# Optimization experiments

Hardware: AMD Instinct MI355X
Metric: run time of the kernel (lower is better)

Reference implementation:

```python
import jax, jax.numpy as jnp
import numpy as np
import math

B, S, D, H, DFF, L = 8, 1024, 512, 8, 2048, 4
DK = D // H
EPS = 1e-5
NEG = -1e32


def _sinusoidal_pe(s, d):
    pos = np.arange(s)[:, None].astype(np.float32)
    div = np.exp(np.arange(0, d, 2).astype(np.float32) * (-math.log(10000.0) / d))
    pe = np.zeros((s, d), np.float32)
    pe[:, 0::2] = np.sin(pos * div)
    pe[:, 1::2] = np.cos(pos * div)
    return jnp.asarray(pe)


def setup_inputs() -> dict:
    key = jax.random.key(0)
    ks = jax.random.split(key, 20)
    sd = 0.02
    inp = {
        "q_embed_data": jax.random.normal(ks[0], (B, S, D), jnp.float32),
        "qa_embed_data": jax.random.normal(ks[1], (B, S, D), jnp.float32),
        "pe": _sinusoidal_pe(S, D),
        # stacked per-layer params (leading dim L). kq_same=1 -> q uses Wk.
        "Wk": sd * jax.random.normal(ks[2], (L, D, D), jnp.float32),
        "bk": jnp.zeros((L, D), jnp.float32),
        "Wv": sd * jax.random.normal(ks[3], (L, D, D), jnp.float32),
        "bv": jnp.zeros((L, D), jnp.float32),
        "Wo": sd * jax.random.normal(ks[4], (L, D, D), jnp.float32),
        "bo": jnp.zeros((L, D), jnp.float32),
        "ln1_s": jnp.ones((L, D), jnp.float32),
        "ln1_b": jnp.zeros((L, D), jnp.float32),
        "W1": sd * jax.random.normal(ks[5], (L, D, DFF), jnp.float32),
        "b1": jnp.zeros((L, DFF), jnp.float32),
        "W2": sd * jax.random.normal(ks[6], (L, DFF, D), jnp.float32),
        "b2": jnp.zeros((L, D), jnp.float32),
        "ln2_s": jnp.ones((L, D), jnp.float32),
        "ln2_b": jnp.zeros((L, D), jnp.float32),
    }
    return inp


def _layernorm(z, s, b):
    m = z.mean(-1, keepdims=True)
    v = ((z - m) ** 2).mean(-1, keepdims=True)
    return (z - m) / jnp.sqrt(v + EPS) * s + b


def _forward(q_embed_data, qa_embed_data, pe, Wk, bk, Wv, bv, Wo, bo,
             ln1_s, ln1_b, W1, b1, W2, b2, ln2_s, ln2_b):
    x = q_embed_data + pe[None, :, :]
    y = qa_embed_data + pe[None, :, :]  # values source stays fixed across blocks
    allowed = jnp.tril(jnp.ones((S, S), bool), -1)  # strictly-causal: attend only to j < i
    row_keep = (jnp.arange(S) > 0).astype(x.dtype)[None, None, :, None]  # zero_pad row 0

    def heads(z, W, b):
        return (z @ W + b).reshape(B, S, H, DK).transpose(0, 2, 1, 3)  # [B,H,S,DK]

    def step(xc, p):
        wk, bk_, wv, bv_, wo, bo_, s1, b1n, w1, b1f, w2, b2f, s2, b2n = p
        q = heads(xc, wk, bk_)  # kq_same: q via k_linear
        k = heads(xc, wk, bk_)
        v = heads(y, wv, bv_)
        sc = jnp.einsum('bhid,bhjd->bhij', q, k) / math.sqrt(DK)
        att = jax.nn.softmax(jnp.where(allowed, sc, NEG), axis=-1) * row_keep
        o = jnp.einsum('bhij,bhjd->bhid', att, v).transpose(0, 2, 1, 3).reshape(B, S, D)
        x1 = _layernorm(xc + (o @ wo + bo_), s1, b1n)
        f = jax.nn.relu(x1 @ w1 + b1f) @ w2 + b2f
        x2 = _layernorm(x1 + f, s2, b2n)
        return x2, None

    out, _ = jax.lax.scan(step, x, (Wk, bk, Wv, bv, Wo, bo, ln1_s, ln1_b, W1, b1, W2, b2, ln2_s, ln2_b))
    return out


def reference(q_embed_data, qa_embed_data, pe, Wk, bk, Wv, bv, Wo, bo,
              ln1_s, ln1_b, W1, b1, W2, b2, ln2_s, ln2_b):
    return _forward(q_embed_data, qa_embed_data, pe, Wk, bk, Wv, bv, Wo, bo,
                    ln1_s, ln1_b, W1, b1, W2, b2, ln2_s, ln2_b)
```

## Files before the change

### kernel.cpp

```cpp
#include <hip/hip_runtime.h>
#include <stdint.h>

typedef __attribute__((ext_vector_type(8))) __bf16 bf16x8;
typedef __attribute__((ext_vector_type(4))) float f32x4;
typedef __attribute__((ext_vector_type(4))) unsigned int u32x4;

constexpr int B = 8, S = 1024, D = 512, H = 8, DFF = 2048, L = 4, DK = 64;
constexpr int MR = B * S;

__device__ __forceinline__ unsigned short f2bf(float f) {
    union { float f; unsigned u; } v; v.f = f;
    unsigned u = v.u;
    u += 0x7fffu + ((u >> 16) & 1u);
    return (unsigned short)(u >> 16);
}

__device__ __forceinline__ void gload_lds16(const void* g, void* l) {
    __builtin_amdgcn_global_load_lds(
        (const __attribute__((address_space(1))) void*)g,
        (__attribute__((address_space(3))) void*)l, 16, 0, 0);
}

__global__ __launch_bounds__(256) void add_pe_kernel(
    const float* __restrict__ qe, const float* __restrict__ qa,
    const float* __restrict__ pe, float* __restrict__ x_f32,
    unsigned short* __restrict__ x_bf, unsigned short* __restrict__ y_bf) {
    int gid = blockIdx.x * 256 + threadIdx.x;
    int base = gid * 4;
    int po = base & (S * D - 1);
    float4 p = *(const float4*)(pe + po);
    float4 a = *(const float4*)(qe + base);
    float4 q = *(const float4*)(qa + base);
    float4 xv = make_float4(a.x + p.x, a.y + p.y, a.z + p.z, a.w + p.w);
    float4 yv = make_float4(q.x + p.x, q.y + p.y, q.z + p.z, q.w + p.w);
    *(float4*)(x_f32 + base) = xv;
    ushort4 xb; xb.x = f2bf(xv.x); xb.y = f2bf(xv.y); xb.z = f2bf(xv.z); xb.w = f2bf(xv.w);
    ushort4 yb; yb.x = f2bf(yv.x); yb.y = f2bf(yv.y); yb.z = f2bf(yv.z); yb.w = f2bf(yv.w);
    *(ushort4*)(x_bf + base) = xb;
    *(ushort4*)(y_bf + base) = yb;
}

__global__ __launch_bounds__(256) void wtrans_kernel(
    const float* __restrict__ src, unsigned short* __restrict__ dst, int K, int N) {
    __shared__ float t[64][65];
    src += (size_t)blockIdx.z * K * N;
    dst += (size_t)blockIdx.z * K * N;
    int n0 = blockIdx.x * 64, k0 = blockIdx.y * 64;
    int tid = threadIdx.x;
    int r = tid >> 4, c4 = (tid & 15) * 4;
    #pragma unroll
    for (int rr = 0; rr < 64; rr += 16) {
        float4 v = *(const float4*)(src + (size_t)(k0 + r + rr) * N + n0 + c4);
        t[r + rr][c4] = v.x; t[r + rr][c4 + 1] = v.y;
        t[r + rr][c4 + 2] = v.z; t[r + rr][c4 + 3] = v.w;
    }
    __syncthreads();
    int n = tid >> 2, kc = (tid & 3) * 16;
    ushort4 o[4];
    #pragma unroll
    for (int g = 0; g < 4; g++) {
        o[g].x = f2bf(t[kc + g * 4 + 0][n]);
        o[g].y = f2bf(t[kc + g * 4 + 1][n]);
        o[g].z = f2bf(t[kc + g * 4 + 2][n]);
        o[g].w = f2bf(t[kc + g * 4 + 3][n]);
    }
    unsigned short* dp = dst + (size_t)(n0 + n) * K + k0 + kc;
    #pragma unroll
    for (int g = 0; g < 4; g++) *(ushort4*)(dp + g * 4) = o[g];
}

template<int BN, bool RELU, bool RESID, bool OUT_F32, bool OUT_BF16, bool OUT_VT>
__global__ __launch_bounds__(256) void gemm_kernel(
    const unsigned short* __restrict__ A, const unsigned short* __restrict__ Bt,
    const float* __restrict__ bias, const float* __restrict__ resid,
    float* __restrict__ out_f32, unsigned short* __restrict__ out_bf,
    int M, int N, int K) {
    constexpr int MT = (BN == 128) ? 4 : 2;
    constexpr int WROWS = (BN == 128) ? 64 : 32;
    __shared__ unsigned short a_lds[128 * 32];
    __shared__ unsigned short b_lds[BN * 32];

    const int tid = threadIdx.x;
    const int lane = tid & 63, wid = tid >> 6;
    const int wm = (BN == 128) ? (wid >> 1) : wid;
    const int wn = (BN == 128) ? (wid & 1) : 0;
    const int l15 = lane & 15, quad = lane >> 4;
    const int m0 = blockIdx.x * 128, n0 = blockIdx.y * BN;

    f32x4 acc[MT][4];
    #pragma unroll
    for (int i = 0; i < MT; i++)
        #pragma unroll
        for (int j = 0; j < 4; j++) { f32x4 z = {0.f, 0.f, 0.f, 0.f}; acc[i][j] = z; }

    const int c0 = wid * 128 + lane, c1 = c0 + 64;
    const int r0 = c0 >> 2, kga0 = (c0 & 3) ^ ((r0 >> 1) & 3);
    const int r1 = c1 >> 2, kga1 = (c1 & 3) ^ ((r1 >> 1) & 3);
    const unsigned short* aP0 = A + (size_t)(m0 + r0) * K + kga0 * 8;
    const unsigned short* aP1 = A + (size_t)(m0 + r1) * K + kga1 * 8;
    unsigned short* aL0 = a_lds + wid * 1024;
    unsigned short* aL1 = aL0 + 512;

    const unsigned short *bP0, *bP1;
    unsigned short *bL0, *bL1;
    if (BN == 128) {
        bP0 = Bt + (size_t)(n0 + r0) * K + kga0 * 8;
        bP1 = Bt + (size_t)(n0 + r1) * K + kga1 * 8;
        bL0 = b_lds + wid * 1024;
        bL1 = bL0 + 512;
    } else {
        int cb = tid, rb = cb >> 2, kgb = (cb & 3) ^ ((rb >> 1) & 3);
        bP0 = Bt + (size_t)(n0 + rb) * K + kgb * 8;
        bP1 = nullptr;
        bL0 = b_lds + wid * 512;
        bL1 = nullptr;
    }

    for (int k0 = 0; k0 < K; k0 += 32) {
        gload_lds16(aP0 + k0, aL0);
        gload_lds16(aP1 + k0, aL1);
        gload_lds16(bP0 + k0, bL0);
        if (BN == 128) gload_lds16(bP1 + k0, bL1);
        __syncthreads();

        bf16x8 af[MT], bfv[4];
        #pragma unroll
        for (int mt = 0; mt < MT; mt++) {
            int row = wm * WROWS + mt * 16 + l15;
            af[mt] = *(const bf16x8*)&a_lds[row * 32 + ((quad ^ ((row >> 1) & 3)) * 8)];
        }
        #pragma unroll
        for (int nt = 0; nt < 4; nt++) {
            int row = wn * 64 + nt * 16 + l15;
            bfv[nt] = *(const bf16x8*)&b_lds[row * 32 + ((quad ^ ((row >> 1) & 3)) * 8)];
        }
        #pragma unroll
        for (int mt = 0; mt < MT; mt++)
            #pragma unroll
            for (int nt = 0; nt < 4; nt++)
                acc[mt][nt] = __builtin_amdgcn_mfma_f32_16x16x32_bf16(af[mt], bfv[nt], acc[mt][nt], 0, 0, 0);
        __syncthreads();
    }

    #pragma unroll
    for (int nt = 0; nt < 4; nt++) {
        int col = n0 + wn * 64 + nt * 16 + l15;
        float bv = bias[col];
        #pragma unroll
        for (int mt = 0; mt < MT; mt++) {
            int row0 = m0 + wm * WROWS + mt * 16 + quad * 4;
            if (OUT_VT) {
                int hh = col >> 6, d = col & 63;
                int bb = row0 >> 10, s0 = row0 & 1023;
                ushort4 o;
                o.x = f2bf(acc[mt][nt][0] + bv);
                o.y = f2bf(acc[mt][nt][1] + bv);
                o.z = f2bf(acc[mt][nt][2] + bv);
                o.w = f2bf(acc[mt][nt][3] + bv);
                *(ushort4*)(out_bf + ((size_t)(bb * H + hh) * DK + d) * S + s0) = o;
            } else {
                #pragma unroll
                for (int r = 0; r < 4; r++) {
                    int row = row0 + r;
                    float v = acc[mt][nt][r] + bv;
                    if (RESID) v += resid[(size_t)row * N + col];
                    if (RELU) v = fmaxf(v, 0.f);
                    size_t o = (size_t)row * N + col;
                    if (OUT_F32) out_f32[o] = v;
                    if (OUT_BF16) out_bf[o] = f2bf(v);
                }
            }
        }
    }
}

__global__ __launch_bounds__(256) void ln_kernel(
    const float* __restrict__ in, const float* __restrict__ gamma,
    const float* __restrict__ beta, float* __restrict__ out_f32,
    unsigned short* __restrict__ out_bf) {
    __shared__ float red[8];
    int row = blockIdx.x, tid = threadIdx.x;
    const float* p = in + (size_t)row * D;
    float2 v = *(const float2*)(p + tid * 2);
    float s = v.x + v.y;
    float q = v.x * v.x + v.y * v.y;
    #pragma unroll
    for (int off = 32; off > 0; off >>= 1) {
        s += __shfl_xor(s, off);
        q += __shfl_xor(q, off);
    }
    int wid = tid >> 6, lane = tid & 63;
    if (lane == 0) { red[wid] = s; red[4 + wid] = q; }
    __syncthreads();
    s = red[0] + red[1] + red[2] + red[3];
    q = red[4] + red[5] + red[6] + red[7];
    float mean = s * (1.f / D);
    float var = q * (1.f / D) - mean * mean;
    float inv = rsqrtf(var + 1e-5f);
    int c = tid * 2;
    float2 g = *(const float2*)(gamma + c);
    float2 bb = *(const float2*)(beta + c);
    float o0 = (v.x - mean) * inv * g.x + bb.x;
    float o1 = (v.y - mean) * inv * g.y + bb.y;
    *(float2*)(out_f32 + (size_t)row * D + c) = make_float2(o0, o1);
    ushort2 ob; ob.x = f2bf(o0); ob.y = f2bf(o1);
    *(ushort2*)(out_bf + (size_t)row * D + c) = ob;
}

__device__ __forceinline__ void load_kfrag(const unsigned short* kbase, int kt,
                                           int l15, int quad, bf16x8 (&kf)[4][2]) {
    #pragma unroll
    for (int mt = 0; mt < 4; mt++) {
        const unsigned short* kr = kbase + (size_t)(kt * 64 + mt * 16 + l15) * D;
        kf[mt][0] = *(const bf16x8*)(kr + quad * 8);
        kf[mt][1] = *(const bf16x8*)(kr + 32 + quad * 8);
    }
}
__device__ __forceinline__ void load_vfrag(const unsigned short* vbase, int kt,
                                           int l15, int quad, bf16x8 (&vf)[4][2]) {
    #pragma unroll
    for (int mt = 0; mt < 4; mt++) {
        const unsigned short* vr = vbase + (size_t)(mt * 16 + l15) * S + kt * 64;
        vf[mt][0] = *(const bf16x8*)(vr + quad * 8);
        vf[mt][1] = *(const bf16x8*)(vr + 32 + quad * 8);
    }
}

__global__ __launch_bounds__(64, 2) void attn_part_kernel(
    const unsigned short* __restrict__ qk, const unsigned short* __restrict__ vt,
    float* __restrict__ part_o, float* __restrict__ part_ml) {
    __shared__ unsigned short p_lds[32 * 72];

    int bx = blockIdx.x;
    int slot = 47 - (bx >> 6);
    int head = bx & 63;
    int b = head >> 3, h = head & 7;
    int lane = threadIdx.x;
    int l15 = lane & 15, quad = lane >> 4;

    int t, ck0, ck1;
    if (slot < 16)      { t = slot;      ck0 = 0;       ck1 = (t >> 1) + 1; }
    else if (slot < 32) { t = slot;      int nt = (t >> 1) + 1; ck0 = 0;       ck1 = nt >> 1; }
    else                { t = slot - 16; int nt = (t >> 1) + 1; ck0 = nt >> 1; ck1 = nt; }

    const int rowbase = b * S, colbase = h * DK;
    const unsigned short* kbase = qk + (size_t)rowbase * D + colbase;
    const unsigned short* vbase = vt + (size_t)(b * H + h) * (DK * S);

    bf16x8 qf[2][2];
    #pragma unroll
    for (int u = 0; u < 2; u++) {
        const unsigned short* qrow =
            qk + (size_t)(rowbase + t * 32 + u * 16 + l15) * D + colbase;
        qf[u][0] = *(const bf16x8*)(qrow + quad * 8);
        qf[u][1] = *(const bf16x8*)(qrow + 32 + quad * 8);
    }

    float m_r[2] = {-1e30f, -1e30f}, l_r[2] = {0.f, 0.f};
    f32x4 o_acc[2][4];
    #pragma unroll
    for (int u = 0; u < 2; u++)
        #pragma unroll
        for (int i = 0; i < 4; i++) { f32x4 z = {0.f, 0.f, 0.f, 0.f}; o_acc[u][i] = z; }

    auto process = [&](int kt, bf16x8 (&kf)[4][2], bf16x8 (&vf)[4][2]) {
        #pragma unroll
        for (int u = 0; u < 2; u++) {
            const int qbase = t * 32 + u * 16;
            if (kt * 64 >= qbase + 16) continue;
            const int gi = qbase + l15;

            f32x4 s_acc[4];
            #pragma unroll
            for (int mt = 0; mt < 4; mt++) {
                if (kt * 64 + mt * 16 < qbase + 16) {
                    f32x4 a = {0.f, 0.f, 0.f, 0.f};
                    a = __builtin_amdgcn_mfma_f32_16x16x32_bf16(kf[mt][0], qf[u][0], a, 0, 0, 0);
                    a = __builtin_amdgcn_mfma_f32_16x16x32_bf16(kf[mt][1], qf[u][1], a, 0, 0, 0);
                    s_acc[mt] = a;
                }
            }

            float p[4][4];
            float mx = -1e30f;
            #pragma unroll
            for (int mt = 0; mt < 4; mt++) {
                if (kt * 64 + mt * 16 < qbase + 16) {
                    #pragma unroll
                    for (int r = 0; r < 4; r++) {
                        int gj = kt * 64 + mt * 16 + quad * 4 + r;
                        float val = s_acc[mt][r] * 0.125f;
                        if (gj >= gi) val = -1e30f;
                        p[mt][r] = val;
                        mx = fmaxf(mx, val);
                    }
                }
            }
            mx = fmaxf(mx, __shfl_xor(mx, 16));
            mx = fmaxf(mx, __shfl_xor(mx, 32));
            float m_new = fmaxf(m_r[u], mx);
            float alpha = __expf(m_r[u] - m_new);
            float ls = 0.f;
            #pragma unroll
            for (int mt = 0; mt < 4; mt++) {
                bool live = kt * 64 + mt * 16 < qbase + 16;
                #pragma unroll
                for (int r = 0; r < 4; r++) {
                    float pv = live ? __expf(p[mt][r] - m_new) : 0.f;
                    p[mt][r] = pv;
                    ls += pv;
                }
            }
            ls += __shfl_xor(ls, 16);
            ls += __shfl_xor(ls, 32);
            l_r[u] = l_r[u] * alpha + ls;
            m_r[u] = m_new;

            const int ql = u * 16 + l15;
            #pragma unroll
            for (int mt = 0; mt < 4; mt++) {
                uint2 w;
                w.x = (unsigned)f2bf(p[mt][0]) | ((unsigned)f2bf(p[mt][1]) << 16);
                w.y = (unsigned)f2bf(p[mt][2]) | ((unsigned)f2bf(p[mt][3]) << 16);
                *(uint2*)&p_lds[ql * 72 + mt * 16 + quad * 4] = w;
            }
            bf16x8 pb0 = *(const bf16x8*)&p_lds[ql * 72 + quad * 8];
            bf16x8 pb1 = *(const bf16x8*)&p_lds[ql * 72 + 32 + quad * 8];

            #pragma unroll
            for (int mt = 0; mt < 4; mt++)
                #pragma unroll
                for (int r = 0; r < 4; r++)
                    o_acc[u][mt][r] *= alpha;
            #pragma unroll
            for (int mt = 0; mt < 4; mt++) {
                o_acc[u][mt] = __builtin_amdgcn_mfma_f32_16x16x32_bf16(vf[mt][0], pb0, o_acc[u][mt], 0, 0, 0);
                o_acc[u][mt] = __builtin_amdgcn_mfma_f32_16x16x32_bf16(vf[mt][1], pb1, o_acc[u][mt], 0, 0, 0);
            }
        }
    };

    bf16x8 ka[4][2], kb[4][2], va[4][2];
    load_kfrag(kbase, ck0, l15, quad, ka);
    int kt = ck0;
    while (true) {
        load_vfrag(vbase, kt, l15, quad, va);
        if (kt + 1 < ck1) load_kfrag(kbase, kt + 1, l15, quad, kb);
        process(kt, ka, va);
        if (++kt >= ck1) break;
        load_vfrag(vbase, kt, l15, quad, va);
        if (kt + 1 < ck1) load_kfrag(kbase, kt + 1, l15, quad, ka);
        process(kt, kb, va);
        if (++kt >= ck1) break;
    }

    int p = head * 48 + slot;
    if (quad == 0) {
        #pragma unroll
        for (int u = 0; u < 2; u++) {
            part_ml[(size_t)p * 64 + u * 16 + l15] = m_r[u];
            part_ml[(size_t)p * 64 + 32 + u * 16 + l15] = l_r[u];
        }
    }
    float* po = part_o + (size_t)p * 2048;
    #pragma unroll
    for (int u = 0; u < 2; u++)
        #pragma unroll
        for (int mt = 0; mt < 4; mt++)
            #pragma unroll
            for (int r = 0; r < 4; r++)
                po[(mt * 16 + quad * 4 + r) * 32 + u * 16 + l15] = o_acc[u][mt][r];
}

__global__ __launch_bounds__(256) void attn_combine_kernel(
    const float* __restrict__ part_o, const float* __restrict__ part_ml,
    unsigned short* __restrict__ ob) {
    int bx = blockIdx.x;
    int t = bx & 31, head = bx >> 5;
    int b = head >> 3, h = head & 7;
    int tid = threadIdx.x;
    int q = tid >> 3, dg = (tid & 7) * 8;
    int p0 = head * 48 + t;
    bool two = (t >= 16);
    int p1 = head * 48 + t + 16;

    float m0 = part_ml[(size_t)p0 * 64 + q];
    float l0 = part_ml[(size_t)p0 * 64 + 32 + q];
    float w0 = 1.f, w1 = 0.f, ldenom = l0;
    if (two) {
        float m1 = part_ml[(size_t)p1 * 64 + q];
        float l1 = part_ml[(size_t)p1 * 64 + 32 + q];
        float M = fmaxf(m0, m1);
        w0 = __expf(m0 - M);
        w1 = __expf(m1 - M);
        ldenom = l0 * w0 + l1 * w1;
    }
    float inv = (ldenom > 0.f) ? 1.f / ldenom : 0.f;
    int si = t * 32 + q;
    if (si == 0) inv = 0.f;

    const float* po0 = part_o + (size_t)p0 * 2048;
    const float* po1 = part_o + (size_t)p1 * 2048;
    unsigned short out[8];
    #pragma unroll
    for (int i = 0; i < 8; i++) {
        int d = dg + i;
        float v = po0[d * 32 + q] * w0;
        if (two) v += po1[d * 32 + q] * w1;
        out[i] = f2bf(v * inv);
    }
    unsigned short* dst = ob + (size_t)(b * S + si) * D + h * DK + dg;
    *(u32x4*)dst = *(const u32x4*)out;
}

extern "C" void kernel_launch(void* const* d_in, const int* in_sizes, int n_in,
                              void* d_out, int out_size, void* d_ws, size_t ws_size,
                              hipStream_t stream) {
    (void)in_sizes; (void)n_in; (void)out_size; (void)ws_size;
    const float* qe  = (const float*)d_in[0];
    const float* qa  = (const float*)d_in[1];
    const float* pe  = (const float*)d_in[2];
    const float* Wk  = (const float*)d_in[3];
    const float* bk  = (const float*)d_in[4];
    const float* Wv  = (const float*)d_in[5];
    const float* bv  = (const float*)d_in[6];
    const float* Wo  = (const float*)d_in[7];
    const float* bo  = (const float*)d_in[8];
    const float* l1s = (const float*)d_in[9];
    const float* l1b = (const float*)d_in[10];
    const float* W1  = (const float*)d_in[11];
    const float* b1  = (const float*)d_in[12];
    const float* W2  = (const float*)d_in[13];
    const float* b2  = (const float*)d_in[14];
    const float* l2s = (const float*)d_in[15];
    const float* l2b = (const float*)d_in[16];

    char* w = (char*)d_ws;
    float* x_f32  = (float*)w;           w += (size_t)MR * D * 4;
    float* t_f32  = (float*)w;           w += (size_t)MR * D * 4;
    float* x1_f32 = (float*)w;           w += (size_t)MR * D * 4;
    unsigned short* x_bf  = (unsigned short*)w; w += (size_t)MR * D * 2;
    unsigned short* y_bf  = (unsigned short*)w; w += (size_t)MR * D * 2;
    unsigned short* qk_bf = (unsigned short*)w; w += (size_t)MR * D * 2;
    unsigned short* vt_bf = (unsigned short*)w; w += (size_t)MR * D * 2;
    unsigned short* o_bf  = (unsigned short*)w; w += (size_t)MR * D * 2;
    unsigned short* x1_bf = (unsigned short*)w; w += (size_t)MR * D * 2;
    unsigned short* h_bf  = (unsigned short*)w; w += (size_t)MR * DFF * 2;
    unsigned short* wkT = (unsigned short*)w;   w += (size_t)L * D * D * 2;
    unsigned short* wvT = (unsigned short*)w;   w += (size_t)L * D * D * 2;
    unsigned short* woT = (unsigned short*)w;   w += (size_t)L * D * D * 2;
    unsigned short* w1T = (unsigned short*)w;   w += (size_t)L * D * DFF * 2;
    unsigned short* w2T = (unsigned short*)w;   w += (size_t)L * DFF * D * 2;
    float* part_o  = (float*)w;                 w += (size_t)3072 * 2048 * 4;
    float* part_ml = (float*)w;                 w += (size_t)3072 * 64 * 4;

    add_pe_kernel<<<MR * D / 4 / 256, 256, 0, stream>>>(qe, qa, pe, x_f32, x_bf, y_bf);
    wtrans_kernel<<<dim3(8, 8, L), 256, 0, stream>>>(Wk, wkT, D, D);
    wtrans_kernel<<<dim3(8, 8, L), 256, 0, stream>>>(Wv, wvT, D, D);
    wtrans_kernel<<<dim3(8, 8, L), 256, 0, stream>>>(Wo, woT, D, D);
    wtrans_kernel<<<dim3(32, 8, L), 256, 0, stream>>>(W1, w1T, D, DFF);
    wtrans_kernel<<<dim3(8, 32, L), 256, 0, stream>>>(W2, w2T, DFF, D);

    dim3 g512(64, 8), g2048(64, 16);
    for (int l = 0; l < L; l++) {
        gemm_kernel<64, false, false, false, true, false><<<g512, 256, 0, stream>>>(
            x_bf, wkT + (size_t)l * D * D, bk + l * D, nullptr, nullptr, qk_bf, MR, D, D);
        gemm_kernel<64, false, false, false, false, true><<<g512, 256, 0, stream>>>(
            y_bf, wvT + (size_t)l * D * D, bv + l * D, nullptr, nullptr, vt_bf, MR, D, D);
        attn_part_kernel<<<48 * 64, 64, 0, stream>>>(qk_bf, vt_bf, part_o, part_ml);
        attn_combine_kernel<<<64 * 32, 256, 0, stream>>>(part_o, part_ml, o_bf);
        gemm_kernel<64, false, true, true, false, false><<<g512, 256, 0, stream>>>(
            o_bf, woT + (size_t)l * D * D, bo + l * D, x_f32, t_f32, nullptr, MR, D, D);
        ln_kernel<<<MR, 256, 0, stream>>>(t_f32, l1s + l * D, l1b + l * D, x1_f32, x1_bf);
        gemm_kernel<128, true, false, false, true, false><<<g2048, 256, 0, stream>>>(
            x1_bf, w1T + (size_t)l * D * DFF, b1 + l * DFF, nullptr, nullptr, h_bf, MR, DFF, D);
        gemm_kernel<64, false, true, true, false, false><<<g512, 256, 0, stream>>>(
            h_bf, w2T + (size_t)l * DFF * D, b2 + l * D, x1_f32, t_f32, nullptr, MR, D, DFF);
        float* xo = (l == L - 1) ? (float*)d_out : x_f32;
        ln_kernel<<<MR, 256, 0, stream>>>(t_f32, l2s + l * D, l2b + l * D, xo, x_bf);
    }
}
```

Measured before the change: 875.5 us.

## Double GEMM K-tile to 64 and streamline attention softmax with exp2

The GEMM now stages 64-wide K slices per iteration with an 8-way XOR swizzle, halving barrier and loop overhead per MFMA. The attention kernel computes softmax in the base-2 domain with a folded scale and skips causal masking on off-diagonal tiles. It also packs probabilities to bf16 by truncation while accumulating the row sum from those truncated values. This doubles GEMM LDS usage and slightly changes rounding of attention probabilities.

Measured after the change: 835.3 us. 1.05x faster.

```diff
diff --git a/kernel.cpp b/kernel.cpp
--- a/kernel.cpp
+++ b/kernel.cpp
@@ -77,8 +77,9 @@
     int M, int N, int K) {
     constexpr int MT = (BN == 128) ? 4 : 2;
     constexpr int WROWS = (BN == 128) ? 64 : 32;
-    __shared__ unsigned short a_lds[128 * 32];
-    __shared__ unsigned short b_lds[BN * 32];
+    constexpr int BRND = (BN == 128) ? 4 : 2;
+    __shared__ unsigned short a_lds[128 * 64];
+    __shared__ unsigned short b_lds[BN * 64];
 
     const int tid = threadIdx.x;
     const int lane = tid & 63, wid = tid >> 6;
@@ -93,52 +94,54 @@
         #pragma unroll
         for (int j = 0; j < 4; j++) { f32x4 z = {0.f, 0.f, 0.f, 0.f}; acc[i][j] = z; }
 
-    const int c0 = wid * 128 + lane, c1 = c0 + 64;
-    const int r0 = c0 >> 2, kga0 = (c0 & 3) ^ ((r0 >> 1) & 3);
-    const int r1 = c1 >> 2, kga1 = (c1 & 3) ^ ((r1 >> 1) & 3);
-    const unsigned short* aP0 = A + (size_t)(m0 + r0) * K + kga0 * 8;
-    const unsigned short* aP1 = A + (size_t)(m0 + r1) * K + kga1 * 8;
-    unsigned short* aL0 = a_lds + wid * 1024;
-    unsigned short* aL1 = aL0 + 512;
-
-    const unsigned short *bP0, *bP1;
-    unsigned short *bL0, *bL1;
-    if (BN == 128) {
-        bP0 = Bt + (size_t)(n0 + r0) * K + kga0 * 8;
-        bP1 = Bt + (size_t)(n0 + r1) * K + kga1 * 8;
-        bL0 = b_lds + wid * 1024;
-        bL1 = bL0 + 512;
-    } else {
-        int cb = tid, rb = cb >> 2, kgb = (cb & 3) ^ ((rb >> 1) & 3);
-        bP0 = Bt + (size_t)(n0 + rb) * K + kgb * 8;
-        bP1 = nullptr;
-        bL0 = b_lds + wid * 512;
-        bL1 = nullptr;
-    }
-
-    for (int k0 = 0; k0 < K; k0 += 32) {
-        gload_lds16(aP0 + k0, aL0);
-        gload_lds16(aP1 + k0, aL1);
-        gload_lds16(bP0 + k0, bL0);
-        if (BN == 128) gload_lds16(bP1 + k0, bL1);
+    const unsigned short* aP[4];
+    unsigned short* aL[4];
+    #pragma unroll
+    for (int j = 0; j < 4; j++) {
+        int c = wid * 256 + j * 64 + lane;
+        int r = c >> 3, slot = c & 7, kg = slot ^ (r & 7);
+        aP[j] = A + (size_t)(m0 + r) * K + kg * 8;
+        aL[j] = a_lds + (size_t)(wid * 256 + j * 64) * 8;
+    }
+    const unsigned short* bP[BRND];
+    unsigned short* bL[BRND];
+    #pragma unroll
+    for (int j = 0; j < BRND; j++) {
+        int c = wid * (BRND * 64) + j * 64 + lane;
+        int r = c >> 3, slot = c & 7, kg = slot ^ (r & 7);
+        bP[j] = Bt + (size_t)(n0 + r) * K + kg * 8;
+        bL[j] = b_lds + (size_t)(wid * (BRND * 64) + j * 64) * 8;
+    }
+
+    for (int k0 = 0; k0 < K; k0 += 64) {
+        #pragma unroll
+        for (int j = 0; j < 4; j++) gload_lds16(aP[j] + k0, aL[j]);
+        #pragma unroll
+        for (int j = 0; j < BRND; j++) gload_lds16(bP[j] + k0, bL[j]);
         __syncthreads();
 
-        bf16x8 af[MT], bfv[4];
+        bf16x8 af[MT][2], bfv[4][2];
         #pragma unroll
         for (int mt = 0; mt < MT; mt++) {
             int row = wm * WROWS + mt * 16 + l15;
-            af[mt] = *(const bf16x8*)&a_lds[row * 32 + ((quad ^ ((row >> 1) & 3)) * 8)];
+            #pragma unroll
+            for (int kh = 0; kh < 2; kh++)
+                af[mt][kh] = *(const bf16x8*)&a_lds[row * 64 + (((kh * 4 + quad) ^ (row & 7)) * 8)];
         }
         #pragma unroll
         for (int nt = 0; nt < 4; nt++) {
             int row = wn * 64 + nt * 16 + l15;
-            bfv[nt] = *(const bf16x8*)&b_lds[row * 32 + ((quad ^ ((row >> 1) & 3)) * 8)];
+            #pragma unroll
+            for (int kh = 0; kh < 2; kh++)
+                bfv[nt][kh] = *(const bf16x8*)&b_lds[row * 64 + (((kh * 4 + quad) ^ (row & 7)) * 8)];
         }
         #pragma unroll
         for (int mt = 0; mt < MT; mt++)
             #pragma unroll
-            for (int nt = 0; nt < 4; nt++)
-                acc[mt][nt] = __builtin_amdgcn_mfma_f32_16x16x32_bf16(af[mt], bfv[nt], acc[mt][nt], 0, 0, 0);
+            for (int nt = 0; nt < 4; nt++) {
+                acc[mt][nt] = __builtin_amdgcn_mfma_f32_16x16x32_bf16(af[mt][0], bfv[nt][0], acc[mt][nt], 0, 0, 0);
+                acc[mt][nt] = __builtin_amdgcn_mfma_f32_16x16x32_bf16(af[mt][1], bfv[nt][1], acc[mt][nt], 0, 0, 0);
+            }
         __syncthreads();
     }
 
@@ -229,7 +232,9 @@
 __global__ __launch_bounds__(64, 2) void attn_part_kernel(
     const unsigned short* __restrict__ qk, const unsigned short* __restrict__ vt,
     float* __restrict__ part_o, float* __restrict__ part_ml) {
-    __shared__ unsigned short p_lds[32 * 72];
+    __shared__ unsigned p_u32[32 * 36];
+    constexpr float C = 0.18033688011112042f;
+    const float NEGINF = -__builtin_huge_valf();
 
     int bx = blockIdx.x;
     int slot = 47 - (bx >> 6);
@@ -263,81 +268,100 @@
         #pragma unroll
         for (int i = 0; i < 4; i++) { f32x4 z = {0.f, 0.f, 0.f, 0.f}; o_acc[u][i] = z; }
 
-    auto process = [&](int kt, bf16x8 (&kf)[4][2], bf16x8 (&vf)[4][2]) {
+    auto process = [&](int kt, bf16x8 (&kf)[4][2], bf16x8 (&vf)[4][2], bool diag) {
+        f32x4 s[2][4];
         #pragma unroll
         for (int u = 0; u < 2; u++) {
-            const int qbase = t * 32 + u * 16;
-            if (kt * 64 >= qbase + 16) continue;
-            const int gi = qbase + l15;
-
-            f32x4 s_acc[4];
+            const int qb = t * 32 + u * 16;
             #pragma unroll
             for (int mt = 0; mt < 4; mt++) {
-                if (kt * 64 + mt * 16 < qbase + 16) {
+                if (!diag || (kt * 64 + mt * 16 < qb + 16)) {
                     f32x4 a = {0.f, 0.f, 0.f, 0.f};
                     a = __builtin_amdgcn_mfma_f32_16x16x32_bf16(kf[mt][0], qf[u][0], a, 0, 0, 0);
                     a = __builtin_amdgcn_mfma_f32_16x16x32_bf16(kf[mt][1], qf[u][1], a, 0, 0, 0);
-                    s_acc[mt] = a;
+                    s[u][mt] = a;
+                } else {
+                    f32x4 a = {NEGINF, NEGINF, NEGINF, NEGINF};
+                    s[u][mt] = a;
                 }
             }
-
-            float p[4][4];
-            float mx = -1e30f;
-            #pragma unroll
-            for (int mt = 0; mt < 4; mt++) {
-                if (kt * 64 + mt * 16 < qbase + 16) {
+        }
+        if (diag) {
+            #pragma unroll
+            for (int u = 0; u < 2; u++) {
+                const int gi = t * 32 + u * 16 + l15;
+                #pragma unroll
+                for (int mt = 0; mt < 4; mt++)
                     #pragma unroll
                     for (int r = 0; r < 4; r++) {
                         int gj = kt * 64 + mt * 16 + quad * 4 + r;
-                        float val = s_acc[mt][r] * 0.125f;
-                        if (gj >= gi) val = -1e30f;
-                        p[mt][r] = val;
-                        mx = fmaxf(mx, val);
+                        s[u][mt][r] = (gj >= gi) ? NEGINF : s[u][mt][r];
                     }
-                }
             }
+        }
+        float mn[2], al[2];
+        #pragma unroll
+        for (int u = 0; u < 2; u++) {
+            float mx = -3e38f;
+            #pragma unroll
+            for (int mt = 0; mt < 4; mt++)
+                #pragma unroll
+                for (int r = 0; r < 4; r++) mx = fmaxf(mx, s[u][mt][r]);
             mx = fmaxf(mx, __shfl_xor(mx, 16));
             mx = fmaxf(mx, __shfl_xor(mx, 32));
-            float m_new = fmaxf(m_r[u], mx);
-            float alpha = __expf(m_r[u] - m_new);
-            float ls = 0.f;
+            float m_new = fmaxf(m_r[u], mx * C);
+            al[u] = exp2f(m_r[u] - m_new);
+            mn[u] = m_new;
+        }
+        float ls[2] = {0.f, 0.f};
+        #pragma unroll
+        for (int u = 0; u < 2; u++) {
+            const int ql = u * 16 + l15;
             #pragma unroll
             for (int mt = 0; mt < 4; mt++) {
-                bool live = kt * 64 + mt * 16 < qbase + 16;
-                #pragma unroll
-                for (int r = 0; r < 4; r++) {
-                    float pv = live ? __expf(p[mt][r] - m_new) : 0.f;
-                    p[mt][r] = pv;
-                    ls += pv;
-                }
+                unsigned a0 = __builtin_bit_cast(unsigned, exp2f(fmaf(s[u][mt][0], C, -mn[u])));
+                unsigned a1 = __builtin_bit_cast(unsigned, exp2f(fmaf(s[u][mt][1], C, -mn[u])));
+                unsigned a2 = __builtin_bit_cast(unsigned, exp2f(fmaf(s[u][mt][2], C, -mn[u])));
+                unsigned a3 = __builtin_bit_cast(unsigned, exp2f(fmaf(s[u][mt][3], C, -mn[u])));
+                p_u32[ql * 36 + mt * 8 + quad * 2]     = (a0 >> 16) | (a1 & 0xffff0000u);
+                p_u32[ql * 36 + mt * 8 + quad * 2 + 1] = (a2 >> 16) | (a3 & 0xffff0000u);
+                float q0 = __builtin_bit_cast(float, a0 & 0xffff0000u);
+                float q1 = __builtin_bit_cast(float, a1 & 0xffff0000u);
+                float q2 = __builtin_bit_cast(float, a2 & 0xffff0000u);
+                float q3 = __builtin_bit_cast(float, a3 & 0xffff0000u);
+                ls[u] += (q0 + q1) + (q2 + q3);
             }
-            ls += __shfl_xor(ls, 16);
-            ls += __shfl_xor(ls, 32);
-            l_r[u] = l_r[u] * alpha + ls;
-            m_r[u] = m_new;
-
+        }
+        #pragma unroll
+        for (int u = 0; u < 2; u++) {
+            ls[u] += __shfl_xor(ls[u], 16);
+            ls[u] += __shfl_xor(ls[u], 32);
+            l_r[u] = l_r[u] * al[u] + ls[u];
+            m_r[u] = mn[u];
+        }
+        bf16x8 pb[2][2];
+        #pragma unroll
+        for (int u = 0; u < 2; u++) {
             const int ql = u * 16 + l15;
-            #pragma unroll
-            for (int mt = 0; mt < 4; mt++) {
-                uint2 w;
-                w.x = (unsigned)f2bf(p[mt][0]) | ((unsigned)f2bf(p[mt][1]) << 16);
-                w.y = (unsigned)f2bf(p[mt][2]) | ((unsigned)f2bf(p[mt][3]) << 16);
-                *(uint2*)&p_lds[ql * 72 + mt * 16 + quad * 4] = w;
-            }
-            bf16x8 pb0 = *(const bf16x8*)&p_lds[ql * 72 + quad * 8];
-            bf16x8 pb1 = *(const bf16x8*)&p_lds[ql * 72 + 32 + quad * 8];
-
+            u32x4 d0 = *(const u32x4*)&p_u32[ql * 36 + quad * 4];
+            u32x4 d1 = *(const u32x4*)&p_u32[ql * 36 + 16 + quad * 4];
+            pb[u][0] = __builtin_bit_cast(bf16x8, d0);
+            pb[u][1] = __builtin_bit_cast(bf16x8, d1);
+        }
+        #pragma unroll
+        for (int u = 0; u < 2; u++)
             #pragma unroll
             for (int mt = 0; mt < 4; mt++)
                 #pragma unroll
                 for (int r = 0; r < 4; r++)
-                    o_acc[u][mt][r] *= alpha;
+                    o_acc[u][mt][r] *= al[u];
+        #pragma unroll
+        for (int u = 0; u < 2; u++)
             #pragma unroll
             for (int mt = 0; mt < 4; mt++) {
-                o_acc[u][mt] = __builtin_amdgcn_mfma_f32_16x16x32_bf16(vf[mt][0], pb0, o_acc[u][mt], 0, 0, 0);
-                o_acc[u][mt] = __builtin_amdgcn_mfma_f32_16x16x32_bf16(vf[mt][1], pb1, o_acc[u][mt], 0, 0, 0);
+                o_acc[u][mt] = __builtin_amdgcn_mfma_f32_16x16x32_bf16(vf[mt][0], pb[u][0], o_acc[u][mt], 0, 0, 0);
+                o_acc[u][mt] = __builtin_amdgcn_mfma_f32_16x16x32_bf16(vf[mt][1], pb[u][1], o_acc[u][mt], 0, 0, 0);
             }
-        }
     };
 
     bf16x8 ka[4][2], kb[4][2], va[4][2];
@@ -346,11 +370,11 @@
     while (true) {
         load_vfrag(vbase, kt, l15, quad, va);
         if (kt + 1 < ck1) load_kfrag(kbase, kt + 1, l15, quad, kb);
-        process(kt, ka, va);
+        process(kt, ka, va, 2 * kt + 2 > t);
         if (++kt >= ck1) break;
         load_vfrag(vbase, kt, l15, quad, va);
         if (kt + 1 < ck1) load_kfrag(kbase, kt + 1, l15, quad, ka);
-        process(kt, kb, va);
+        process(kt, kb, va, 2 * kt + 2 > t);
         if (++kt >= ck1) break;
     }
 
@@ -391,8 +415,8 @@
         float m1 = part_ml[(size_t)p1 * 64 + q];
         float l1 = part_ml[(size_t)p1 * 64 + 32 + q];
         float M = fmaxf(m0, m1);
-        w0 = __expf(m0 - M);
-        w1 = __expf(m1 - M);
+        w0 = exp2f(m0 - M);
+        w1 = exp2f(m1 - M);
         ldenom = l0 * w0 + l1 * w1;
     }
     float inv = (ldenom > 0.f) ? 1.f / ldenom : 0.f;
```
